# Kernel optimization log

Hardware: AMD Instinct MI355X
Metric: run time of the kernel (lower is better)

Reference implementation:

```python
import jax, jax.numpy as jnp
import numpy as np

N = 50000      # nodes
E = 1600000    # edges (avg degree 32)
D = 128        # node feature dim
C = 10         # classes
BN_EPS = 1e-5


def _w(k, shape, fan_in):
    lim = 1.0 / np.sqrt(fan_in)
    return jax.random.uniform(k, shape, jnp.float32, -lim, lim)


def setup_inputs() -> dict:
    key = jax.random.key(0)
    ks = jax.random.split(key, 16)
    inp = {}
    inp["x"] = jax.random.normal(ks[0], (N, D), jnp.float32)
    inp["edge_attr"] = jax.random.normal(ks[1], (E, 1), jnp.float32)
    inp["edge_index"] = jax.random.randint(ks[2], (2, E), 0, N)
    # edge-attr projection Linear(1, D) (D_n > D_e branch)
    inp["lin_w"] = _w(ks[3], (1, D), 1)
    inp["lin_b"] = jnp.zeros((D,), jnp.float32)
    # conv1 nn: MLP([D, D]) = Linear + ReLU + BatchNorm1d
    inp["w1"] = _w(ks[4], (D, D), D); inp["b1"] = jnp.zeros((D,)); inp["g1"] = jnp.ones((D,)); inp["be1"] = jnp.zeros((D,))
    # conv2 nn: MLP([D, 64])
    inp["w2"] = _w(ks[5], (D, 64), D); inp["b2"] = jnp.zeros((64,)); inp["g2"] = jnp.ones((64,)); inp["be2"] = jnp.zeros((64,))
    # lin1: MLP([D+64, 96])
    inp["w3"] = _w(ks[6], (D + 64, 96), D + 64); inp["b3"] = jnp.zeros((96,)); inp["g3"] = jnp.ones((96,)); inp["be3"] = jnp.zeros((96,))
    # mlp1: MLP([96, 96, C])
    inp["w4"] = _w(ks[7], (96, 96), 96); inp["b4"] = jnp.zeros((96,)); inp["g4"] = jnp.ones((96,)); inp["be4"] = jnp.zeros((96,))
    inp["w5"] = _w(ks[8], (96, C), 96); inp["b5"] = jnp.zeros((C,)); inp["g5"] = jnp.ones((C,)); inp["be5"] = jnp.zeros((C,))
    return inp


def _bn(h, g, b):
    # BatchNorm1d training-mode: batch statistics, biased variance
    m = h.mean(axis=0)
    v = h.var(axis=0)
    return g * (h - m) * jax.lax.rsqrt(v + BN_EPS) + b


def _mlp_layer(h, w, b, g, be):
    # nn.Sequential(Linear, ReLU, BatchNorm1d)
    return _bn(jax.nn.relu(h @ w + b), g, be)


def reference(x, edge_attr, edge_index, lin_w, lin_b,
              w1, b1, g1, be1, w2, b2, g2, be2,
              w3, b3, g3, be3, w4, b4, g4, be4,
              w5, b5, g5, be5):
    # project scalar edge features to node dim (D_n > D_e branch)
    e = edge_attr @ lin_w + lin_b  # [E, D]
    src, dst = edge_index[0], edge_index[1]

    def gine(h, w, b, g, be):
        # GINEConv (eps=0): nn(x_i + sum_j relu(x_j + e_ji))
        msg = jax.nn.relu(h[src] + e)                      # [E, D]
        aggr = jax.ops.segment_sum(msg, dst, num_segments=N)  # [N, D]
        return _mlp_layer(h + aggr, w, b, g, be)

    x1 = gine(x, w1, b1, g1, be1)    # [N, D]
    x2 = gine(x1, w2, b2, g2, be2)   # [N, 64]
    h = _mlp_layer(jnp.concatenate([x1, x2], axis=1), w3, b3, g3, be3)  # [N, 96]
    h = _mlp_layer(h, w4, b4, g4, be4)  # [N, 96]
    h = _mlp_layer(h, w5, b5, g5, be5)  # [N, C]
    return h
```

## Files before the change

kernel.cpp:

```cpp
#include <hip/hip_runtime.h>
#include <hip/hip_fp16.h>

static constexpr float BN_EPS = 1e-5f;

using half8 = __attribute__((ext_vector_type(8))) _Float16;
using f32x4 = __attribute__((ext_vector_type(4))) float;

__device__ __forceinline__ ushort f2h(float f) {
    return __half_as_ushort(__float2half(f));
}
__device__ __forceinline__ float2 h2f2(uint u) {
    __half2 h = *reinterpret_cast<__half2*>(&u);
    return __half22float2(h);
}
__device__ __forceinline__ float h2f1(ushort u) {
    __half h = *reinterpret_cast<__half*>(&u);
    return __half2float(h);
}

__global__ __launch_bounds__(256) void cvt_f16(
    const float* __restrict__ in, ushort* __restrict__ out, int n4)
{
    int i = blockIdx.x * 256 + threadIdx.x;
    const int stride = gridDim.x * 256;
    for (; i < n4; i += stride) {
        const float4 v = ((const float4*)in)[i];
        ushort4 u;
        u.x = f2h(v.x); u.y = f2h(v.y); u.z = f2h(v.z); u.w = f2h(v.w);
        ((ushort4*)out)[i] = u;
    }
}

__device__ __forceinline__ void pack_store(ushort* dst, int M, int k, int c, float v)
{
    const int kc = k >> 5, kk = k & 31, ct = c >> 4;
    const int lane = (c & 15) | ((kk >> 3) << 4);
    const int j = kk & 7;
    dst[((size_t)(kc * (M / 16) + ct) * 64 + lane) * 8 + j] = f2h(v);
}

__global__ __launch_bounds__(256) void pack_all(
    const float* __restrict__ w1, const float* __restrict__ w2,
    const float* __restrict__ w3, const float* __restrict__ w4,
    const float* __restrict__ w5, const float* __restrict__ b5,
    ushort* __restrict__ Wp, float* __restrict__ b5p, float* __restrict__ sums)
{
    int t = blockIdx.x * 256 + threadIdx.x;
    if (t < 16384) { pack_store(Wp, 128, t / 128, t % 128, w1[t]); return; }
    t -= 16384;
    if (t < 8192) { pack_store(Wp + 16384, 64, t / 64, t % 64, w2[t]); return; }
    t -= 8192;
    if (t < 18432) { pack_store(Wp + 24576, 96, t / 96, t % 96, w3[t]); return; }
    t -= 18432;
    if (t < 9216) { pack_store(Wp + 43008, 96, t / 96, t % 96, w4[t]); return; }
    t -= 9216;
    if (t < 1536) {
        const int k = t / 16, c = t % 16;
        pack_store(Wp + 52224, 16, k, c, (c < 10) ? w5[k * 10 + c] : 0.f);
        return;
    }
    t -= 1536;
    if (t < 16) { b5p[t] = (t < 10) ? b5[t] : 0.f; return; }
    t -= 16;
    if (t < 1280) sums[t] = 0.f;
}

__device__ inline int wave_incl_scan(int v, int lane)
{
#pragma unroll
    for (int s = 1; s < 64; s <<= 1) {
        const int t = __shfl_up(v, s, 64);
        if (lane >= s) v += t;
    }
    return v;
}

__global__ __launch_bounds__(1024) void scan1(
    const int* __restrict__ cnt, int* __restrict__ off, int* __restrict__ bsum, int n)
{
    __shared__ int wsum[16];
    const int tid = threadIdx.x, lane = tid & 63, wid = tid >> 6;
    const int i = blockIdx.x * 1024 + tid;
    const int v = (i < n) ? cnt[i] : 0;
    const int incl = wave_incl_scan(v, lane);
    if (lane == 63) wsum[wid] = incl;
    __syncthreads();
    if (wid == 0) {
        int wv = (lane < 16) ? wsum[lane] : 0;
        wv = wave_incl_scan(wv, lane);
        if (lane < 16) wsum[lane] = wv;
    }
    __syncthreads();
    const int excl = (wid > 0 ? wsum[wid - 1] : 0) + incl - v;
    if (i < n) off[i] = excl;
    if (tid == 1023) bsum[blockIdx.x] = wsum[15];
}

__global__ __launch_bounds__(64) void scan2(int* __restrict__ bsum, int nb)
{
    const int lane = threadIdx.x;
    int carry = 0;
    for (int base = 0; base < nb; base += 64) {
        const int idx = base + lane;
        const int v = (idx < nb) ? bsum[idx] : 0;
        const int incl = wave_incl_scan(v, lane);
        if (idx < nb) bsum[idx] = carry + incl - v;
        carry += __shfl(incl, 63, 64);
    }
}

__global__ __launch_bounds__(1024) void scan3(
    int* __restrict__ off, const int* __restrict__ bsum, int n)
{
    const int i = blockIdx.x * 1024 + threadIdx.x;
    if (i < n) off[i] += bsum[blockIdx.x];
}

__global__ __launch_bounds__(256) void hist_blocks(
    const int* __restrict__ dst, int* __restrict__ H, int E, int NB, int NBLK)
{
    __shared__ int h[512];
    for (int i = threadIdx.x; i < NB; i += 256) h[i] = 0;
    __syncthreads();
    const int chunk = (E + NBLK - 1) / NBLK;
    const int beg = blockIdx.x * chunk;
    const int end = min(beg + chunk, E);
    for (int i = beg + threadIdx.x; i < end; i += 256)
        atomicAdd(&h[dst[i] >> 7], 1);
    __syncthreads();
    for (int i = threadIdx.x; i < NB; i += 256)
        H[(size_t)i * NBLK + blockIdx.x] = h[i];
}

__global__ __launch_bounds__(256) void scatter_coarse(
    const int* __restrict__ src, const int* __restrict__ dst,
    const float* __restrict__ ea, const int* __restrict__ H,
    int2* __restrict__ tmp, int E, int NB, int NBLK)
{
    __shared__ int h[512];
    for (int i = threadIdx.x; i < NB; i += 256)
        h[i] = H[(size_t)i * NBLK + blockIdx.x];
    __syncthreads();
    const int chunk = (E + NBLK - 1) / NBLK;
    const int beg = blockIdx.x * chunk;
    const int end = min(beg + chunk, E);
    for (int i = beg + threadIdx.x; i < end; i += 256) {
        const int d = dst[i];
        const int pos = atomicAdd(&h[d >> 7], 1);
        tmp[pos] = make_int2(src[i] | ((d & 127) << 20), __float_as_int(ea[i]));
    }
}

__global__ __launch_bounds__(256) void fill_fine2(
    const int2* __restrict__ tmp, const int* __restrict__ H,
    int* __restrict__ off, uint* __restrict__ edges, int N, int E, int NBLK)
{
    __shared__ int cnt[128];
    __shared__ int wtot;
    const int b = blockIdx.x;
    const int base = b * 128;
    const int tid = threadIdx.x;
    const int lo = H[(size_t)b * NBLK];
    const int hi = (b + 1 < (int)gridDim.x) ? H[(size_t)(b + 1) * NBLK] : E;
    if (tid < 128) cnt[tid] = 0;
    __syncthreads();
    for (int i = lo + tid; i < hi; i += 256)
        atomicAdd(&cnt[(tmp[i].x >> 20) & 127], 1);
    __syncthreads();
    int excl = 0;
    if (tid < 128) {
        const int v = cnt[tid];
        const int incl = wave_incl_scan(v, tid & 63);
        if (tid == 63) wtot = incl;
        excl = incl - v;
    }
    __syncthreads();
    if (tid >= 64 && tid < 128) excl += wtot;
    if (tid < 128) {
        const int o = lo + excl;
        if (base + tid < N) off[base + tid] = o;
        cnt[tid] = o;
    }
    if (b == 0 && tid == 0) off[N] = E;
    __syncthreads();
    for (int i = lo + tid; i < hi; i += 256) {
        const int2 p = tmp[i];
        const int dl = (p.x >> 20) & 127;
        const int pos = atomicAdd(&cnt[dl], 1);
        edges[pos] = (uint)(p.x & 0xFFFF) | ((uint)f2h(__int_as_float(p.y)) << 16);
    }
}

template<bool AFF>
__global__ __launch_bounds__(256) void gine_aggr(
    const ushort* __restrict__ xh, const int* __restrict__ off,
    const uint* __restrict__ edges, const float* __restrict__ lw,
    const float* __restrict__ lb, const float* __restrict__ su,
    const float* __restrict__ qu, const float* __restrict__ g,
    const float* __restrict__ be, float invN,
    ushort* __restrict__ outh, int N)
{
    const int q = threadIdx.x & 31;
    const int node = blockIdx.x * 8 + (threadIdx.x >> 5);
    if (node >= N) return;
    const float4 lw4 = ((const float4*)lw)[q];
    const float4 lb4 = ((const float4*)lb)[q];
    float4 sc4, sh4;
    if constexpr (AFF) {
        const float4 sv = ((const float4*)su)[q];
        const float4 qv = ((const float4*)qu)[q];
        const float4 gv = ((const float4*)g)[q];
        const float4 bv = ((const float4*)be)[q];
        float4 m;
        m.x = sv.x * invN; m.y = sv.y * invN; m.z = sv.z * invN; m.w = sv.w * invN;
        sc4.x = gv.x * rsqrtf(qv.x * invN - m.x * m.x + BN_EPS);
        sc4.y = gv.y * rsqrtf(qv.y * invN - m.y * m.y + BN_EPS);
        sc4.z = gv.z * rsqrtf(qv.z * invN - m.z * m.z + BN_EPS);
        sc4.w = gv.w * rsqrtf(qv.w * invN - m.w * m.w + BN_EPS);
        sh4.x = bv.x - m.x * sc4.x; sh4.y = bv.y - m.y * sc4.y;
        sh4.z = bv.z - m.z * sc4.z; sh4.w = bv.w - m.w * sc4.w;
    }
    float4 s;
    {
        const uint2 u = ((const uint2*)(xh + (size_t)node * 128))[q];
        float2 f0 = h2f2(u.x), f1 = h2f2(u.y);
        if constexpr (AFF) {
            f0.x = fmaf(f0.x, sc4.x, sh4.x); f0.y = fmaf(f0.y, sc4.y, sh4.y);
            f1.x = fmaf(f1.x, sc4.z, sh4.z); f1.y = fmaf(f1.y, sc4.w, sh4.w);
        }
        s.x = f0.x; s.y = f0.y; s.z = f1.x; s.w = f1.y;
    }
    int p = off[node];
    const int pend = off[node + 1];
    if (p < pend) {
        uint e = edges[p];
        uint2 u = ((const uint2*)(xh + (size_t)(e & 0xFFFFu) * 128))[q];
        for (++p; p < pend; ++p) {
            const uint en = edges[p];
            const uint2 un = ((const uint2*)(xh + (size_t)(en & 0xFFFFu) * 128))[q];
            const float a = h2f1((ushort)(e >> 16));
            float2 f0 = h2f2(u.x), f1 = h2f2(u.y);
            if constexpr (AFF) {
                f0.x = fmaf(f0.x, sc4.x, sh4.x); f0.y = fmaf(f0.y, sc4.y, sh4.y);
                f1.x = fmaf(f1.x, sc4.z, sh4.z); f1.y = fmaf(f1.y, sc4.w, sh4.w);
            }
            s.x += fmaxf(fmaf(a, lw4.x, lb4.x) + f0.x, 0.f);
            s.y += fmaxf(fmaf(a, lw4.y, lb4.y) + f0.y, 0.f);
            s.z += fmaxf(fmaf(a, lw4.z, lb4.z) + f1.x, 0.f);
            s.w += fmaxf(fmaf(a, lw4.w, lb4.w) + f1.y, 0.f);
            e = en; u = un;
        }
        const float a = h2f1((ushort)(e >> 16));
        float2 f0 = h2f2(u.x), f1 = h2f2(u.y);
        if constexpr (AFF) {
            f0.x = fmaf(f0.x, sc4.x, sh4.x); f0.y = fmaf(f0.y, sc4.y, sh4.y);
            f1.x = fmaf(f1.x, sc4.z, sh4.z); f1.y = fmaf(f1.y, sc4.w, sh4.w);
        }
        s.x += fmaxf(fmaf(a, lw4.x, lb4.x) + f0.x, 0.f);
        s.y += fmaxf(fmaf(a, lw4.y, lb4.y) + f0.y, 0.f);
        s.z += fmaxf(fmaf(a, lw4.z, lb4.z) + f1.x, 0.f);
        s.w += fmaxf(fmaf(a, lw4.w, lb4.w) + f1.y, 0.f);
    }
    ushort4 o;
    o.x = f2h(s.x); o.y = f2h(s.y); o.z = f2h(s.z); o.w = f2h(s.w);
    ((ushort4*)(outh + (size_t)node * 128))[q] = o;
}

__device__ __forceinline__ half8 affine_h8(
    half8 a, const float* sc, const float* sh, int k)
{
    const float4 c0 = *(const float4*)(sc + k), c1 = *(const float4*)(sc + k + 4);
    const float4 d0 = *(const float4*)(sh + k), d1 = *(const float4*)(sh + k + 4);
    half8 r;
    r[0] = (_Float16)fmaf((float)a[0], c0.x, d0.x);
    r[1] = (_Float16)fmaf((float)a[1], c0.y, d0.y);
    r[2] = (_Float16)fmaf((float)a[2], c0.z, d0.z);
    r[3] = (_Float16)fmaf((float)a[3], c0.w, d0.w);
    r[4] = (_Float16)fmaf((float)a[4], c1.x, d1.x);
    r[5] = (_Float16)fmaf((float)a[5], c1.y, d1.y);
    r[6] = (_Float16)fmaf((float)a[6], c1.z, d1.z);
    r[7] = (_Float16)fmaf((float)a[7], c1.w, d1.w);
    return r;
}

template<int K, int KS, int M, bool YH, bool AF1, bool AF2>
__global__ __launch_bounds__(256) void gemm_mfma(
    const ushort* __restrict__ A1, const ushort* __restrict__ A2,
    const float* __restrict__ su1, const float* __restrict__ sq1_,
    const float* __restrict__ g1, const float* __restrict__ be1,
    const float* __restrict__ su2, const float* __restrict__ sq2_,
    const float* __restrict__ g2, const float* __restrict__ be2,
    const ushort* __restrict__ Wp, const float* __restrict__ bias,
    void* __restrict__ Yv, float* __restrict__ sum, float* __restrict__ sq,
    int N, float invN)
{
    constexpr int NCT = M / 16;
    constexpr int NKC = K / 32;
    __shared__ float redS[4][M];
    __shared__ float redQ[4][M];
    __shared__ float scL[K];
    __shared__ float shL[K];
    const int tid = threadIdx.x;
    if constexpr (AF1 || AF2) {
        for (int i = tid; i < K; i += 256) {
            float s_, q_, g_, b_;
            if (i < KS) { s_ = su1[i]; q_ = sq1_[i]; g_ = g1[i]; b_ = be1[i]; }
            else        { s_ = su2[i - KS]; q_ = sq2_[i - KS]; g_ = g2[i - KS]; b_ = be2[i - KS]; }
            const float m = s_ * invN;
            const float c = g_ * rsqrtf(q_ * invN - m * m + BN_EPS);
            scL[i] = c; shL[i] = b_ - m * c;
        }
        __syncthreads();
    }
    const int w = tid >> 6, l = tid & 63;
    const int col = l & 15, kg = l >> 4;
    const int rowA = blockIdx.x * 64 + w * 16 + col;
    const int rA = (rowA < N) ? rowA : (N - 1);
    f32x4 acc[NCT];
#pragma unroll
    for (int ct = 0; ct < NCT; ++ct) acc[ct] = f32x4{0.f, 0.f, 0.f, 0.f};
#pragma unroll
    for (int kc = 0; kc < NKC; ++kc) {
        const int kbase = kc * 32 + kg * 8;
        half8 a;
        if constexpr (KS < K) {
            if (kbase >= KS) {
                a = *(const half8*)(A2 + (size_t)rA * (K - KS) + (kbase - KS));
                if constexpr (AF2) a = affine_h8(a, scL, shL, kbase);
            } else {
                a = *(const half8*)(A1 + (size_t)rA * KS + kbase);
                if constexpr (AF1) a = affine_h8(a, scL, shL, kbase);
            }
        } else {
            a = *(const half8*)(A1 + (size_t)rA * K + kbase);
            if constexpr (AF1) a = affine_h8(a, scL, shL, kbase);
        }
#pragma unroll
        for (int ct = 0; ct < NCT; ++ct) {
            const half8 wf = *(const half8*)(Wp + ((size_t)(kc * NCT + ct) * 64 + l) * 8);
            acc[ct] = __builtin_amdgcn_mfma_f32_16x16x32_f16(a, wf, acc[ct], 0, 0, 0);
        }
    }
    const int row0 = blockIdx.x * 64 + w * 16 + 4 * kg;
#pragma unroll
    for (int ct = 0; ct < NCT; ++ct) {
        const float bs = bias[ct * 16 + col];
        float sS = 0.f, sQ = 0.f;
#pragma unroll
        for (int r = 0; r < 4; ++r) {
            const int ro = row0 + r;
            if (ro < N) {
                const float o = fmaxf(acc[ct][r] + bs, 0.f);
                if constexpr (YH) ((ushort*)Yv)[(size_t)ro * M + ct * 16 + col] = f2h(o);
                else              ((float*)Yv)[(size_t)ro * M + ct * 16 + col] = o;
                sS += o; sQ = fmaf(o, o, sQ);
            }
        }
        sS += __shfl_xor(sS, 16, 64); sQ += __shfl_xor(sQ, 16, 64);
        sS += __shfl_xor(sS, 32, 64); sQ += __shfl_xor(sQ, 32, 64);
        if (l < 16) { redS[w][ct * 16 + col] = sS; redQ[w][ct * 16 + col] = sQ; }
    }
    __syncthreads();
    for (int i = tid; i < M; i += 256) {
        const float S = redS[0][i] + redS[1][i] + redS[2][i] + redS[3][i];
        const float Q = redQ[0][i] + redQ[1][i] + redQ[2][i] + redQ[3][i];
        unsafeAtomicAdd(&sum[i], S);
        unsafeAtomicAdd(&sq[i], Q);
    }
}

__global__ __launch_bounds__(256) void bn_apply_final(
    const float* __restrict__ Y16, const float* __restrict__ su,
    const float* __restrict__ qu, const float* __restrict__ g5,
    const float* __restrict__ be5, float* __restrict__ out, int total, float invN)
{
    for (int i = blockIdx.x * 256 + threadIdx.x; i < total; i += gridDim.x * 256) {
        const int n = i / 10;
        const int c = i - n * 10;
        const float m = su[c] * invN;
        const float sc = g5[c] * rsqrtf(qu[c] * invN - m * m + BN_EPS);
        const float sh = be5[c] - m * sc;
        out[i] = fmaf(Y16[(size_t)n * 16 + c], sc, sh);
    }
}

extern "C" void kernel_launch(void* const* d_in, const int* in_sizes, int n_in,
                              void* d_out, int out_size, void* d_ws, size_t ws_size,
                              hipStream_t stream)
{
    const float* x   = (const float*)d_in[0];
    const float* ea  = (const float*)d_in[1];
    const int*   ei  = (const int*)d_in[2];
    const float* lw  = (const float*)d_in[3];
    const float* lb  = (const float*)d_in[4];
    const float* w1  = (const float*)d_in[5];
    const float* b1  = (const float*)d_in[6];
    const float* g1  = (const float*)d_in[7];
    const float* be1 = (const float*)d_in[8];
    const float* w2  = (const float*)d_in[9];
    const float* b2  = (const float*)d_in[10];
    const float* g2  = (const float*)d_in[11];
    const float* be2 = (const float*)d_in[12];
    const float* w3  = (const float*)d_in[13];
    const float* b3  = (const float*)d_in[14];
    const float* g3  = (const float*)d_in[15];
    const float* be3 = (const float*)d_in[16];
    const float* w4  = (const float*)d_in[17];
    const float* b4  = (const float*)d_in[18];
    const float* g4  = (const float*)d_in[19];
    const float* be4 = (const float*)d_in[20];
    const float* w5  = (const float*)d_in[21];
    const float* b5  = (const float*)d_in[22];
    const float* g5  = (const float*)d_in[23];
    const float* be5 = (const float*)d_in[24];

    const int N = in_sizes[0] / 128;
    const int E = in_sizes[1];
    const int* src = ei;
    const int* dst = ei + E;
    const float invN = 1.0f / (float)N;

    float* ws = (float*)d_ws;
    ushort* Pa = (ushort*)ws;
    ushort* Pb = (ushort*)(ws + (size_t)N * 64);
    ushort* Pc = (ushort*)(ws + (size_t)N * 128);
    ushort* Pd = (ushort*)(ws + (size_t)N * 160);
    float*  y5 = ws + (size_t)N * 208;
    float*  smallr = ws + (size_t)N * 224;
    float*  sums   = smallr;
    float*  b5p    = smallr + 1280;
    ushort* Wp     = (ushort*)(ws + (size_t)N * 224 + 1296);
    int*    ibase  = (int*)(ws + (size_t)N * 224 + 1296 + 26880);
    int*    H      = ibase;
    int*    bsum   = H + 100160;
    int2*   tmp    = (int2*)(bsum + 128);
    uint*   edges  = (uint*)(tmp + E);
    int*    off    = (int*)(edges + E);
#define SUM(l)   (sums + (l) * 128)
#define SQ(l)    (sums + (5 + (l)) * 128)

    pack_all<<<216, 256, 0, stream>>>(w1, w2, w3, w4, w5, b5, Wp, b5p, sums);
    cvt_f16<<<2048, 256, 0, stream>>>(x, Pa, N * 32);

    const int NB   = (N + 127) / 128;
    const int NBLK = 256;
    const int nH   = NB * NBLK;
    const int nbH  = (nH + 1023) / 1024;
    hist_blocks<<<NBLK, 256, 0, stream>>>(dst, H, E, NB, NBLK);
    scan1<<<nbH, 1024, 0, stream>>>(H, H, bsum, nH);
    scan2<<<1, 64, 0, stream>>>(bsum, nbH);
    scan3<<<nbH, 1024, 0, stream>>>(H, bsum, nH);
    scatter_coarse<<<NBLK, 256, 0, stream>>>(src, dst, ea, H, tmp, E, NB, NBLK);
    fill_fine2<<<NB, 256, 0, stream>>>(tmp, H, off, edges, N, E, NBLK);

    const int gemmGrid = (N + 63) / 64;
    const int aggrGrid = (N + 7) / 8;

    gine_aggr<false><<<aggrGrid, 256, 0, stream>>>(
        Pa, off, edges, lw, lb, nullptr, nullptr, nullptr, nullptr, invN, Pb, N);
    gemm_mfma<128, 128, 128, true, false, false><<<gemmGrid, 256, 0, stream>>>(
        Pb, nullptr, nullptr, nullptr, nullptr, nullptr,
        nullptr, nullptr, nullptr, nullptr,
        Wp, b1, Pa, SUM(0), SQ(0), N, invN);

    gine_aggr<true><<<aggrGrid, 256, 0, stream>>>(
        Pa, off, edges, lw, lb, SUM(0), SQ(0), g1, be1, invN, Pb, N);
    gemm_mfma<128, 128, 64, true, false, false><<<gemmGrid, 256, 0, stream>>>(
        Pb, nullptr, nullptr, nullptr, nullptr, nullptr,
        nullptr, nullptr, nullptr, nullptr,
        Wp + 16384, b2, Pc, SUM(1), SQ(1), N, invN);

    gemm_mfma<192, 128, 96, true, true, true><<<gemmGrid, 256, 0, stream>>>(
        Pa, Pc, SUM(0), SQ(0), g1, be1, SUM(1), SQ(1), g2, be2,
        Wp + 24576, b3, Pb, SUM(2), SQ(2), N, invN);

    gemm_mfma<96, 96, 96, true, true, false><<<gemmGrid, 256, 0, stream>>>(
        Pb, nullptr, SUM(2), SQ(2), g3, be3, nullptr, nullptr, nullptr, nullptr,
        Wp + 43008, b4, Pd, SUM(3), SQ(3), N, invN);

    gemm_mfma<96, 96, 16, false, true, false><<<gemmGrid, 256, 0, stream>>>(
        Pd, nullptr, SUM(3), SQ(3), g4, be4, nullptr, nullptr, nullptr, nullptr,
        Wp + 52224, b5p, y5, SUM(4), SQ(4), N, invN);

    bn_apply_final<<<1024, 256, 0, stream>>>(y5, SUM(4), SQ(4), g5, be5,
                                             (float*)d_out, N * 10, invN);
#undef SUM
#undef SQ
}
```

Measured before the change: 332.2 us.

## Aggregate GINE messages in packed half2 with 16 lanes per node

The neighbor aggregation kernel now does its message math (edge projection, BN affine, ReLU, accumulation) in packed fp16 half2 arithmetic. Each node is handled by 16 lanes with 16-byte gathers instead of 32 lanes with 8-byte gathers, and the edge-attr projection weights are prepacked to half2. The edge CSR build also splits the temporary buffer into a 4-byte packed edge array plus a 1-byte local-dst array, so fp16 conversion happens once in scatter_coarse and the fill stage writes less. The goal is fewer ALU ops and wider memory transactions in the gather-bound aggregation. The cost is accumulating sums of about 32 messages in fp16, which loses precision and could overflow.

```diff
diff --git a/kernel.cpp b/kernel.cpp
--- a/kernel.cpp
+++ b/kernel.cpp
@@ -9,13 +9,17 @@
 __device__ __forceinline__ ushort f2h(float f) {
     return __half_as_ushort(__float2half(f));
 }
-__device__ __forceinline__ float2 h2f2(uint u) {
-    __half2 h = *reinterpret_cast<__half2*>(&u);
-    return __half22float2(h);
-}
-__device__ __forceinline__ float h2f1(ushort u) {
-    __half h = *reinterpret_cast<__half*>(&u);
-    return __half2float(h);
+__device__ __forceinline__ __half2 u2h2(uint u) {
+    union { uint u; __half2 h; } c; c.u = u; return c.h;
+}
+__device__ __forceinline__ uint h22u(__half2 h) {
+    union { uint u; __half2 h; } c; c.h = h; return c.u;
+}
+__device__ __forceinline__ uint pk2(float a, float b) {
+    return (uint)f2h(a) | ((uint)f2h(b) << 16);
+}
+__device__ __forceinline__ uint relu2u(uint u) {
+    return u & ~(((u >> 15) & 0x10001u) * 0xFFFFu);
 }
 
 __global__ __launch_bounds__(256) void cvt_f16(
@@ -43,7 +47,9 @@
     const float* __restrict__ w1, const float* __restrict__ w2,
     const float* __restrict__ w3, const float* __restrict__ w4,
     const float* __restrict__ w5, const float* __restrict__ b5,
-    ushort* __restrict__ Wp, float* __restrict__ b5p, float* __restrict__ sums)
+    const float* __restrict__ lw, const float* __restrict__ lb,
+    ushort* __restrict__ Wp, float* __restrict__ b5p, float* __restrict__ sums,
+    uint* __restrict__ lwh, uint* __restrict__ lbh)
 {
     int t = blockIdx.x * 256 + threadIdx.x;
     if (t < 16384) { pack_store(Wp, 128, t / 128, t % 128, w1[t]); return; }
@@ -62,7 +68,11 @@
     t -= 1536;
     if (t < 16) { b5p[t] = (t < 10) ? b5[t] : 0.f; return; }
     t -= 16;
-    if (t < 1280) sums[t] = 0.f;
+    if (t < 1280) { sums[t] = 0.f; return; }
+    t -= 1280;
+    if (t < 64) { lwh[t] = pk2(lw[2 * t], lw[2 * t + 1]); return; }
+    t -= 64;
+    if (t < 64) { lbh[t] = pk2(lb[2 * t], lb[2 * t + 1]); return; }
 }
 
 __device__ inline int wave_incl_scan(int v, int lane)
@@ -135,7 +145,7 @@
 __global__ __launch_bounds__(256) void scatter_coarse(
     const int* __restrict__ src, const int* __restrict__ dst,
     const float* __restrict__ ea, const int* __restrict__ H,
-    int2* __restrict__ tmp, int E, int NB, int NBLK)
+    uint* __restrict__ tmp_e, uchar* __restrict__ tmp_d, int E, int NB, int NBLK)
 {
     __shared__ int h[512];
     for (int i = threadIdx.x; i < NB; i += 256)
@@ -147,13 +157,15 @@
     for (int i = beg + threadIdx.x; i < end; i += 256) {
         const int d = dst[i];
         const int pos = atomicAdd(&h[d >> 7], 1);
-        tmp[pos] = make_int2(src[i] | ((d & 127) << 20), __float_as_int(ea[i]));
+        tmp_e[pos] = (uint)(src[i] & 0xFFFF) | ((uint)f2h(ea[i]) << 16);
+        tmp_d[pos] = (uchar)(d & 127);
     }
 }
 
 __global__ __launch_bounds__(256) void fill_fine2(
-    const int2* __restrict__ tmp, const int* __restrict__ H,
-    int* __restrict__ off, uint* __restrict__ edges, int N, int E, int NBLK)
+    const uint* __restrict__ tmp_e, const uchar* __restrict__ tmp_d,
+    const int* __restrict__ H, int* __restrict__ off, uint* __restrict__ edges,
+    int N, int E, int NBLK)
 {
     __shared__ int cnt[128];
     __shared__ int wtot;
@@ -165,7 +177,7 @@
     if (tid < 128) cnt[tid] = 0;
     __syncthreads();
     for (int i = lo + tid; i < hi; i += 256)
-        atomicAdd(&cnt[(tmp[i].x >> 20) & 127], 1);
+        atomicAdd(&cnt[tmp_d[i]], 1);
     __syncthreads();
     int excl = 0;
     if (tid < 128) {
@@ -184,86 +196,86 @@
     if (b == 0 && tid == 0) off[N] = E;
     __syncthreads();
     for (int i = lo + tid; i < hi; i += 256) {
-        const int2 p = tmp[i];
-        const int dl = (p.x >> 20) & 127;
+        const int dl = tmp_d[i];
+        const uint pe = tmp_e[i];
         const int pos = atomicAdd(&cnt[dl], 1);
-        edges[pos] = (uint)(p.x & 0xFFFF) | ((uint)f2h(__int_as_float(p.y)) << 16);
+        edges[pos] = pe;
     }
 }
 
 template<bool AFF>
 __global__ __launch_bounds__(256) void gine_aggr(
     const ushort* __restrict__ xh, const int* __restrict__ off,
-    const uint* __restrict__ edges, const float* __restrict__ lw,
-    const float* __restrict__ lb, const float* __restrict__ su,
+    const uint* __restrict__ edges, const uint* __restrict__ lwh,
+    const uint* __restrict__ lbh, const float* __restrict__ su,
     const float* __restrict__ qu, const float* __restrict__ g,
     const float* __restrict__ be, float invN,
     ushort* __restrict__ outh, int N)
 {
-    const int q = threadIdx.x & 31;
-    const int node = blockIdx.x * 8 + (threadIdx.x >> 5);
+    const int q = threadIdx.x & 15;
+    const int node = blockIdx.x * 16 + (threadIdx.x >> 4);
     if (node >= N) return;
-    const float4 lw4 = ((const float4*)lw)[q];
-    const float4 lb4 = ((const float4*)lb)[q];
-    float4 sc4, sh4;
+    __half2 lw[4], lb[4], sc[4], sh[4];
+#pragma unroll
+    for (int i = 0; i < 4; ++i) {
+        lw[i] = u2h2(lwh[q * 4 + i]);
+        lb[i] = u2h2(lbh[q * 4 + i]);
+    }
     if constexpr (AFF) {
-        const float4 sv = ((const float4*)su)[q];
-        const float4 qv = ((const float4*)qu)[q];
-        const float4 gv = ((const float4*)g)[q];
-        const float4 bv = ((const float4*)be)[q];
-        float4 m;
-        m.x = sv.x * invN; m.y = sv.y * invN; m.z = sv.z * invN; m.w = sv.w * invN;
-        sc4.x = gv.x * rsqrtf(qv.x * invN - m.x * m.x + BN_EPS);
-        sc4.y = gv.y * rsqrtf(qv.y * invN - m.y * m.y + BN_EPS);
-        sc4.z = gv.z * rsqrtf(qv.z * invN - m.z * m.z + BN_EPS);
-        sc4.w = gv.w * rsqrtf(qv.w * invN - m.w * m.w + BN_EPS);
-        sh4.x = bv.x - m.x * sc4.x; sh4.y = bv.y - m.y * sc4.y;
-        sh4.z = bv.z - m.z * sc4.z; sh4.w = bv.w - m.w * sc4.w;
-    }
-    float4 s;
+        const int c0 = q * 8;
+#pragma unroll
+        for (int i = 0; i < 4; ++i) {
+            const float2 s2 = *(const float2*)(su + c0 + 2 * i);
+            const float2 q2 = *(const float2*)(qu + c0 + 2 * i);
+            const float2 g2 = *(const float2*)(g + c0 + 2 * i);
+            const float2 b2 = *(const float2*)(be + c0 + 2 * i);
+            const float m0 = s2.x * invN, m1 = s2.y * invN;
+            const float c0f = g2.x * rsqrtf(q2.x * invN - m0 * m0 + BN_EPS);
+            const float c1f = g2.y * rsqrtf(q2.y * invN - m1 * m1 + BN_EPS);
+            sc[i] = u2h2(pk2(c0f, c1f));
+            sh[i] = u2h2(pk2(b2.x - m0 * c0f, b2.y - m1 * c1f));
+        }
+    }
+    __half2 acc[4];
     {
-        const uint2 u = ((const uint2*)(xh + (size_t)node * 128))[q];
-        float2 f0 = h2f2(u.x), f1 = h2f2(u.y);
+        const uint4 u = ((const uint4*)(xh + (size_t)node * 128))[q];
+        acc[0] = u2h2(u.x); acc[1] = u2h2(u.y); acc[2] = u2h2(u.z); acc[3] = u2h2(u.w);
         if constexpr (AFF) {
-            f0.x = fmaf(f0.x, sc4.x, sh4.x); f0.y = fmaf(f0.y, sc4.y, sh4.y);
-            f1.x = fmaf(f1.x, sc4.z, sh4.z); f1.y = fmaf(f1.y, sc4.w, sh4.w);
-        }
-        s.x = f0.x; s.y = f0.y; s.z = f1.x; s.w = f1.y;
-    }
+#pragma unroll
+            for (int i = 0; i < 4; ++i) acc[i] = __hfma2(acc[i], sc[i], sh[i]);
+        }
+    }
+
+    auto proc = [&](uint e, uint4 u) {
+        const __half2 a2 = u2h2((e >> 16) * 0x10001u);
+        uint ua[4] = {u.x, u.y, u.z, u.w};
+#pragma unroll
+        for (int i = 0; i < 4; ++i) {
+            __half2 x2 = u2h2(ua[i]);
+            if constexpr (AFF) x2 = __hfma2(x2, sc[i], sh[i]);
+            __half2 m = __hfma2(a2, lw[i], lb[i]);
+            m = __hadd2(x2, m);
+            m = u2h2(relu2u(h22u(m)));
+            acc[i] = __hadd2(acc[i], m);
+        }
+    };
+
     int p = off[node];
     const int pend = off[node + 1];
     if (p < pend) {
         uint e = edges[p];
-        uint2 u = ((const uint2*)(xh + (size_t)(e & 0xFFFFu) * 128))[q];
+        uint4 u = ((const uint4*)(xh + (size_t)(e & 0xFFFFu) * 128))[q];
         for (++p; p < pend; ++p) {
             const uint en = edges[p];
-            const uint2 un = ((const uint2*)(xh + (size_t)(en & 0xFFFFu) * 128))[q];
-            const float a = h2f1((ushort)(e >> 16));
-            float2 f0 = h2f2(u.x), f1 = h2f2(u.y);
-            if constexpr (AFF) {
-                f0.x = fmaf(f0.x, sc4.x, sh4.x); f0.y = fmaf(f0.y, sc4.y, sh4.y);
-                f1.x = fmaf(f1.x, sc4.z, sh4.z); f1.y = fmaf(f1.y, sc4.w, sh4.w);
-            }
-            s.x += fmaxf(fmaf(a, lw4.x, lb4.x) + f0.x, 0.f);
-            s.y += fmaxf(fmaf(a, lw4.y, lb4.y) + f0.y, 0.f);
-            s.z += fmaxf(fmaf(a, lw4.z, lb4.z) + f1.x, 0.f);
-            s.w += fmaxf(fmaf(a, lw4.w, lb4.w) + f1.y, 0.f);
+            const uint4 un = ((const uint4*)(xh + (size_t)(en & 0xFFFFu) * 128))[q];
+            proc(e, u);
             e = en; u = un;
         }
-        const float a = h2f1((ushort)(e >> 16));
-        float2 f0 = h2f2(u.x), f1 = h2f2(u.y);
-        if constexpr (AFF) {
-            f0.x = fmaf(f0.x, sc4.x, sh4.x); f0.y = fmaf(f0.y, sc4.y, sh4.y);
-            f1.x = fmaf(f1.x, sc4.z, sh4.z); f1.y = fmaf(f1.y, sc4.w, sh4.w);
-        }
-        s.x += fmaxf(fmaf(a, lw4.x, lb4.x) + f0.x, 0.f);
-        s.y += fmaxf(fmaf(a, lw4.y, lb4.y) + f0.y, 0.f);
-        s.z += fmaxf(fmaf(a, lw4.z, lb4.z) + f1.x, 0.f);
-        s.w += fmaxf(fmaf(a, lw4.w, lb4.w) + f1.y, 0.f);
-    }
-    ushort4 o;
-    o.x = f2h(s.x); o.y = f2h(s.y); o.z = f2h(s.z); o.w = f2h(s.w);
-    ((ushort4*)(outh + (size_t)node * 128))[q] = o;
+        proc(e, u);
+    }
+    uint4 o;
+    o.x = h22u(acc[0]); o.y = h22u(acc[1]); o.z = h22u(acc[2]); o.w = h22u(acc[3]);
+    ((uint4*)(outh + (size_t)node * 128))[q] = o;
 }
 
 __device__ __forceinline__ half8 affine_h8(
@@ -429,17 +441,20 @@
     float*  smallr = ws + (size_t)N * 224;
     float*  sums   = smallr;
     float*  b5p    = smallr + 1280;
-    ushort* Wp     = (ushort*)(ws + (size_t)N * 224 + 1296);
-    int*    ibase  = (int*)(ws + (size_t)N * 224 + 1296 + 26880);
+    uint*   lwh    = (uint*)(smallr + 1296);
+    uint*   lbh    = lwh + 64;
+    ushort* Wp     = (ushort*)(smallr + 1424);
+    int*    ibase  = (int*)(smallr + 1424 + 26880);
     int*    H      = ibase;
     int*    bsum   = H + 100160;
-    int2*   tmp    = (int2*)(bsum + 128);
-    uint*   edges  = (uint*)(tmp + E);
+    uint*   tmp_e  = (uint*)(bsum + 128);
+    uchar*  tmp_d  = (uchar*)(tmp_e + E);
+    uint*   edges  = (uint*)(tmp_d + ((E + 3) & ~3));
     int*    off    = (int*)(edges + E);
 #define SUM(l)   (sums + (l) * 128)
 #define SQ(l)    (sums + (5 + (l)) * 128)
 
-    pack_all<<<216, 256, 0, stream>>>(w1, w2, w3, w4, w5, b5, Wp, b5p, sums);
+    pack_all<<<216, 256, 0, stream>>>(w1, w2, w3, w4, w5, b5, lw, lb, Wp, b5p, sums, lwh, lbh);
     cvt_f16<<<2048, 256, 0, stream>>>(x, Pa, N * 32);
 
     const int NB   = (N + 127) / 128;
@@ -450,21 +465,21 @@
     scan1<<<nbH, 1024, 0, stream>>>(H, H, bsum, nH);
     scan2<<<1, 64, 0, stream>>>(bsum, nbH);
     scan3<<<nbH, 1024, 0, stream>>>(H, bsum, nH);
-    scatter_coarse<<<NBLK, 256, 0, stream>>>(src, dst, ea, H, tmp, E, NB, NBLK);
-    fill_fine2<<<NB, 256, 0, stream>>>(tmp, H, off, edges, N, E, NBLK);
+    scatter_coarse<<<NBLK, 256, 0, stream>>>(src, dst, ea, H, tmp_e, tmp_d, E, NB, NBLK);
+    fill_fine2<<<NB, 256, 0, stream>>>(tmp_e, tmp_d, H, off, edges, N, E, NBLK);
 
     const int gemmGrid = (N + 63) / 64;
-    const int aggrGrid = (N + 7) / 8;
+    const int aggrGrid = (N + 15) / 16;
 
     gine_aggr<false><<<aggrGrid, 256, 0, stream>>>(
-        Pa, off, edges, lw, lb, nullptr, nullptr, nullptr, nullptr, invN, Pb, N);
+        Pa, off, edges, lwh, lbh, nullptr, nullptr, nullptr, nullptr, invN, Pb, N);
     gemm_mfma<128, 128, 128, true, false, false><<<gemmGrid, 256, 0, stream>>>(
         Pb, nullptr, nullptr, nullptr, nullptr, nullptr,
         nullptr, nullptr, nullptr, nullptr,
         Wp, b1, Pa, SUM(0), SQ(0), N, invN);
 
     gine_aggr<true><<<aggrGrid, 256, 0, stream>>>(
-        Pa, off, edges, lw, lb, SUM(0), SQ(0), g1, be1, invN, Pb, N);
+        Pa, off, edges, lwh, lbh, SUM(0), SQ(0), g1, be1, invN, Pb, N);
     gemm_mfma<128, 128, 64, true, false, false><<<gemmGrid, 256, 0, stream>>>(
         Pb, nullptr, nullptr, nullptr, nullptr, nullptr,
         nullptr, nullptr, nullptr, nullptr,
```

After: 326.6 us. No clear change (-1.7%).
